# Kernel tuning notes

Hardware: AMD Instinct MI355X
Metric: run time of the kernel (lower is better)

The kernel has to match this reference:

```python
import jax, jax.numpy as jnp
import numpy as np

B, S, H = 1, 2048, 4096
NH, NKV, HD = 32, 8, 128
GROUPS = NH // NKV  # 4
THETA = 10000.0
NEG = -1e9


def setup_inputs() -> dict:
    key = jax.random.key(0)
    k1, k2, k3 = jax.random.split(key, 3)
    hidden_states = jax.random.normal(k1, (B, S, H), dtype=jnp.float32)
    w_qkv = jax.random.normal(k2, (H, (NH + 2 * NKV) * HD), dtype=jnp.float32) * 0.02
    w_o = jax.random.normal(k3, (NH * HD, H), dtype=jnp.float32) * 0.02
    causal = jnp.tril(jnp.ones((S, S), dtype=bool))
    attention_mask = jnp.where(causal, 0.0, NEG).astype(jnp.float32)[None, None]  # [1,1,S,S]
    return {"hidden_states": hidden_states, "w_qkv": w_qkv, "w_o": w_o,
            "attention_mask": attention_mask}


def _rope_freqs(seqlen, head_dim, theta):
    inv = 1.0 / (theta ** (jnp.arange(0, head_dim, 2, dtype=jnp.float32) / head_dim))
    t = jnp.arange(seqlen, dtype=jnp.float32)
    freqs = t[:, None] * inv[None, :]              # [S, HD/2]
    return jnp.cos(freqs), jnp.sin(freqs)


def _apply_rope(x, cos, sin):
    # x: [B,S,heads,HD]; source pairs x[i] with x[i+HD/2] (NeoX rotate-half)
    half = x.shape[-1] // 2
    x1, x2 = x[..., :half], x[..., half:]
    c = cos[None, :, None, :]
    s = sin[None, :, None, :]
    return jnp.concatenate([x1 * c - x2 * s, x1 * s + x2 * c], axis=-1)


def reference(hidden_states, w_qkv, w_o, attention_mask):
    bsz, seqlen, _ = hidden_states.shape
    xqkv = hidden_states @ w_qkv                            # [B,S,(NH+2*NKV)*HD]
    xqkv = xqkv.reshape(bsz, seqlen, NH + 2 * NKV, HD)
    xq = xqkv[:, :, :NH]                                    # [B,S,NH,HD]
    xk = xqkv[:, :, NH:NH + NKV]                            # [B,S,NKV,HD]
    xv = xqkv[:, :, NH + NKV:]                              # [B,S,NKV,HD]

    cos, sin = _rope_freqs(seqlen, HD, THETA)               # start_pos = 0 (prefill)
    xq = _apply_rope(xq, cos, sin)
    xk = _apply_rope(xk, cos, sin)

    # GQA: repeat kv heads to match query heads
    keys = jnp.repeat(xk, GROUPS, axis=2)                   # [B,S,NH,HD]
    values = jnp.repeat(xv, GROUPS, axis=2)

    scores = jnp.einsum('bqhd,bkhd->bhqk', xq, keys) / np.sqrt(HD)
    scores = scores + attention_mask
    probs = jax.nn.softmax(scores.astype(jnp.float32), axis=-1).astype(xq.dtype)
    out = jnp.einsum('bhqk,bkhd->bqhd', probs, values)      # [B,S,NH,HD]
    attention_weight = out.reshape(bsz, seqlen, NH * HD)
    attn_output = attention_weight @ w_o                    # [B,S,H]
    return attn_output
```

## Files before the change

### kernel.cpp

```cpp
#include <hip/hip_runtime.h>

typedef __bf16 bf16_8 __attribute__((ext_vector_type(8)));
typedef float f32x4 __attribute__((ext_vector_type(4)));
typedef unsigned short ushort8v __attribute__((ext_vector_type(8)));
typedef unsigned short ushort4v __attribute__((ext_vector_type(4)));

#define SEQ 2048
#define HDIM 4096
#define NHEADS 32
#define NKVH 8
#define HEADD 128
#define NQKV 6144

__device__ __forceinline__ unsigned short f2bf(float f) {
    unsigned int u = __float_as_uint(f);
    u += 0x7fffu + ((u >> 16) & 1u);
    return (unsigned short)(u >> 16);
}
__device__ __forceinline__ float bf2f(unsigned short v) {
    return __uint_as_float(((unsigned int)v) << 16);
}

#if defined(__has_builtin)
#if __has_builtin(__builtin_amdgcn_exp2f)
#define EXP2(x) __builtin_amdgcn_exp2f(x)
#endif
#endif
#ifndef EXP2
#define EXP2(x) __expf(0.69314718055994531f * (x))
#endif

typedef __attribute__((address_space(1))) void as1_void;
typedef __attribute__((address_space(3))) void as3_void;
__device__ __forceinline__ void gload16(const unsigned short* g, unsigned short* l) {
    __builtin_amdgcn_global_load_lds((as1_void*)g, (as3_void*)l, 16, 0, 0);
}

__global__ void k_f32_to_bf16(const float* __restrict__ in, unsigned short* __restrict__ out, int n) {
    int i = (blockIdx.x * blockDim.x + threadIdx.x) * 4;
    if (i >= n) return;
    float4 v = *reinterpret_cast<const float4*>(in + i);
    ushort4v o = { f2bf(v.x), f2bf(v.y), f2bf(v.z), f2bf(v.w) };
    *reinterpret_cast<ushort4v*>(out + i) = o;
}

__global__ void k_transpose_f32_to_bf16(const float* __restrict__ in, unsigned short* __restrict__ out,
                                        int K, int N) {
    __shared__ unsigned short tile[64][72];
    int k0 = blockIdx.y * 64, n0 = blockIdx.x * 64;
    int t = threadIdx.x;
    int r = t >> 2;
    int cs = (t & 3) * 16;
    int sw = (r >> 4) * 16;
    const float* src = in + (size_t)(k0 + r) * N + n0 + cs;
#pragma unroll
    for (int j = 0; j < 16; j += 4) {
        float4 v = *reinterpret_cast<const float4*>(src + j);
        tile[r][(cs + j + 0) ^ sw] = f2bf(v.x);
        tile[r][(cs + j + 1) ^ sw] = f2bf(v.y);
        tile[r][(cs + j + 2) ^ sw] = f2bf(v.z);
        tile[r][(cs + j + 3) ^ sw] = f2bf(v.w);
    }
    __syncthreads();
    int rr = t >> 2;
    int ks = (t & 3) * 16;
    unsigned short tmp[16];
#pragma unroll
    for (int i = 0; i < 16; i++) tmp[i] = tile[ks + i][rr ^ (((ks + i) >> 4) * 16)];
    unsigned short* dst = out + (size_t)(n0 + rr) * K + k0 + ks;
    *reinterpret_cast<ushort8v*>(dst) = *reinterpret_cast<const ushort8v*>(tmp);
    *reinterpret_cast<ushort8v*>(dst + 8) = *reinterpret_cast<const ushort8v*>(tmp + 8);
}

__global__ void k_transpose_bf16(const unsigned short* __restrict__ in, unsigned short* __restrict__ out,
                                 int inStride, int outStride) {
    __shared__ unsigned short tile[64][72];
    int r0 = blockIdx.y * 64, c0 = blockIdx.x * 64;
    int t = threadIdx.x;
    int r = t >> 2;
    int cs = (t & 3) * 16;
    int csw = cs ^ ((r >> 4) * 16);
    const unsigned short* src = in + (size_t)(r0 + r) * inStride + c0 + cs;
    *reinterpret_cast<ushort8v*>(&tile[r][csw])     = *reinterpret_cast<const ushort8v*>(src);
    *reinterpret_cast<ushort8v*>(&tile[r][csw + 8]) = *reinterpret_cast<const ushort8v*>(src + 8);
    __syncthreads();
    int rr = t >> 2;
    int ks = (t & 3) * 16;
    unsigned short tmp[16];
#pragma unroll
    for (int i = 0; i < 16; i++) tmp[i] = tile[ks + i][rr ^ (((ks + i) >> 4) * 16)];
    unsigned short* dst = out + (size_t)(c0 + rr) * outStride + r0 + ks;
    *reinterpret_cast<ushort8v*>(dst) = *reinterpret_cast<const ushort8v*>(tmp);
    *reinterpret_cast<ushort8v*>(dst + 8) = *reinterpret_cast<const ushort8v*>(tmp + 8);
}


#define STAGE_A(TILE, KH) do { if ((TILE) < NT) {                                        \
    size_t kb_ = (size_t)(TILE) * 128 + (size_t)((KH) * 64);                             \
    gload16((const unsigned short*)(srcA0 + kb_),                                        \
            (unsigned short*)(smem + ((TILE) & 1) * 32768 + (KH) * 16384 + wby));        \
    gload16((const unsigned short*)(srcA1 + kb_),                                        \
            (unsigned short*)(smem + ((TILE) & 1) * 32768 + (KH) * 16384 + 8192 + wby)); \
  } } while (0)

#define STAGE_B(TILE, KH) do { if ((TILE) < NT) {                                        \
    size_t kb_ = (size_t)(TILE) * 128 + (size_t)((KH) * 64);                             \
    gload16((const unsigned short*)(srcB0 + kb_),                                        \
            (unsigned short*)(smem + 65536 + ((TILE) & 1) * 32768 + (KH) * 16384 + wby)); \
    gload16((const unsigned short*)(srcB1 + kb_),                                        \
            (unsigned short*)(smem + 65536 + ((TILE) & 1) * 32768 + (KH) * 16384 + 8192 + wby)); \
  } } while (0)

#define MFMA_ROW(ACCI, AV)                                                                \
    acc[ACCI][0] = __builtin_amdgcn_mfma_f32_16x16x32_bf16(AV, b0, acc[ACCI][0], 0, 0, 0); \
    acc[ACCI][1] = __builtin_amdgcn_mfma_f32_16x16x32_bf16(AV, b1, acc[ACCI][1], 0, 0, 0); \
    acc[ACCI][2] = __builtin_amdgcn_mfma_f32_16x16x32_bf16(AV, b2, acc[ACCI][2], 0, 0, 0); \
    acc[ACCI][3] = __builtin_amdgcn_mfma_f32_16x16x32_bf16(AV, b3, acc[ACCI][3], 0, 0, 0);

#define PHASE(PB, PKH, PMH, DOB, STAGE_STMT, DOVM) do {                                   \
    const char* ab_ = smem + (PB) * 32768 + (PKH) * 16384;                                \
    a0 = *(const bf16_8*)(ab_ + offA[(PMH) * 4 + 0]);                                     \
    a1 = *(const bf16_8*)(ab_ + offA[(PMH) * 4 + 1]);                                     \
    a2 = *(const bf16_8*)(ab_ + offA[(PMH) * 4 + 2]);                                     \
    a3 = *(const bf16_8*)(ab_ + offA[(PMH) * 4 + 3]);                                     \
    if (DOB) {                                                                            \
        const char* bb_ = smem + 65536 + (PB) * 32768 + (PKH) * 16384;                    \
        b0 = *(const bf16_8*)(bb_ + offB[0]);                                             \
        b1 = *(const bf16_8*)(bb_ + offB[1]);                                             \
        b2 = *(const bf16_8*)(bb_ + offB[2]);                                             \
        b3 = *(const bf16_8*)(bb_ + offB[3]);                                             \
    }                                                                                     \
    STAGE_STMT;                                                                           \
    if (DOVM) asm volatile("s_waitcnt vmcnt(8)" ::: "memory");                            \
    __builtin_amdgcn_s_barrier();                                                         \
    __builtin_amdgcn_s_setprio(1);                                                        \
    MFMA_ROW((PMH) * 4 + 0, a0)                                                           \
    MFMA_ROW((PMH) * 4 + 1, a1)                                                           \
    MFMA_ROW((PMH) * 4 + 2, a2)                                                           \
    MFMA_ROW((PMH) * 4 + 3, a3)                                                           \
    __builtin_amdgcn_s_setprio(0);                                                        \
    asm volatile("s_waitcnt lgkmcnt(0)" ::: "memory");                                    \
    __builtin_amdgcn_s_barrier();                                                         \
  } while (0)

template <bool OUT_BF16>
__global__ __launch_bounds__(512, 2) void k_gemm256(
    const unsigned short* __restrict__ A,
    const unsigned short* __restrict__ Bt,
    void* __restrict__ Cv,
    int N, int K)
{
    extern __shared__ char smem[];
    const int NT = K >> 6;
    const int NTN = N >> 8;

    int nwg = gridDim.x;
    int bid = blockIdx.x;
    int cpx = nwg >> 3;
    int sw = (bid & 7) * cpx + (bid >> 3);
    int tm = sw / NTN, tn = sw % NTN;
    int gm0 = tm << 8, gn0 = tn << 8;

    int t = threadIdx.x;
    int w = t >> 6, lane = t & 63;
    int l15 = lane & 15, quad = lane >> 4;
    int wr = w >> 2, wc = w & 3;
    int wby = w << 10;

    int offA[8], offB[4];
#pragma unroll
    for (int mh = 0; mh < 2; mh++)
#pragma unroll
        for (int mi = 0; mi < 4; mi++) {
            int row = wr * 128 + mh * 64 + mi * 16 + l15;
            offA[mh * 4 + mi] = row * 64 + ((quad ^ ((row >> 1) & 3)) << 4);
        }
#pragma unroll
    for (int nj = 0; nj < 4; nj++) {
        int row = wc * 64 + nj * 16 + l15;
        offB[nj] = row * 64 + ((quad ^ ((row >> 1) & 3)) << 4);
    }

    int srow0 = t >> 2;
    int sslot = (t & 3) ^ ((srow0 >> 1) & 3);
    const char* srcA0 = (const char*)A  + ((size_t)(gm0 + srow0)       * K + sslot * 8) * 2;
    const char* srcA1 = (const char*)A  + ((size_t)(gm0 + srow0 + 128) * K + sslot * 8) * 2;
    const char* srcB0 = (const char*)Bt + ((size_t)(gn0 + srow0)       * K + sslot * 8) * 2;
    const char* srcB1 = (const char*)Bt + ((size_t)(gn0 + srow0 + 128) * K + sslot * 8) * 2;

    f32x4 acc[8][4] = {};
    bf16_8 a0, a1, a2, a3, b0, b1, b2, b3;

    STAGE_A(0, 0); STAGE_B(0, 0);
    STAGE_A(0, 1); STAGE_B(0, 1);
    STAGE_A(1, 0); STAGE_B(1, 0);
    asm volatile("s_waitcnt vmcnt(8)" ::: "memory");
    __builtin_amdgcn_s_barrier();

    const int NITER = K >> 7;
    for (int it = 0; it < NITER; ++it) {
        int T1 = 2 * it + 1, T2 = T1 + 1, T3 = T1 + 2;
        PHASE(0, 0, 0, 1, STAGE_A(T1, 1), 0);
        PHASE(0, 0, 1, 0, STAGE_B(T1, 1), 1);
        PHASE(0, 1, 0, 1, STAGE_A(T2, 0), 0);
        PHASE(0, 1, 1, 0, STAGE_B(T2, 0), 1);
        PHASE(1, 0, 0, 1, STAGE_A(T2, 1), 0);
        PHASE(1, 0, 1, 0, STAGE_B(T2, 1), 1);
        PHASE(1, 1, 0, 1, STAGE_A(T3, 0), 0);
        PHASE(1, 1, 1, 0, STAGE_B(T3, 0), 1);
    }

    int crow = gm0 + wr * 128 + quad * 4;
    int ccol = gn0 + wc * 64 + l15;
#pragma unroll
    for (int m8 = 0; m8 < 8; m8++)
#pragma unroll
        for (int nj = 0; nj < 4; nj++)
#pragma unroll
            for (int r = 0; r < 4; r++) {
                size_t idx = (size_t)(crow + m8 * 16 + r) * N + (ccol + nj * 16);
                float v = acc[m8][nj][r];
                if (OUT_BF16) ((unsigned short*)Cv)[idx] = f2bf(v);
                else          ((float*)Cv)[idx] = v;
            }
}

#undef STAGE_A
#undef STAGE_B
#undef MFMA_ROW
#undef PHASE

__global__ void k_rope_split(const unsigned short* __restrict__ qkv,
                             unsigned short* __restrict__ Qb,
                             unsigned short* __restrict__ Kb)
{
    int wid = blockIdx.x * 4 + (threadIdx.x >> 6);
    int lane = threadIdx.x & 63;
    int head = wid % 40;
    int s = wid / 40;
    const unsigned short* src = qkv + (size_t)s * NQKV + head * HEADD;
    float x1 = bf2f(src[lane]);
    float x2 = bf2f(src[lane + 64]);
    float inv = __expf(-(float)lane * 0.14391156831212787f);
    float ang = (float)s * inv;
    float sn, c;
    __sincosf(ang, &sn, &c);
    float o1 = x1 * c - x2 * sn;
    float o2 = x1 * sn + x2 * c;
    unsigned short* dst;
    if (head < 32) {
        const float s2 = 0.12752908270648427f;
        o1 *= s2; o2 *= s2;
        dst = Qb + ((size_t)head * SEQ + s) * HEADD;
    } else {
        dst = Kb + ((size_t)(head - 32) * SEQ + s) * HEADD;
    }
    dst[lane] = f2bf(o1);
    dst[lane + 64] = f2bf(o2);
}

__global__ __launch_bounds__(256, 4) void k_attention(
    const unsigned short* __restrict__ Qb,
    const unsigned short* __restrict__ Kb,
    const unsigned short* __restrict__ Vt,
    unsigned short* __restrict__ Ob)
{
    __shared__ unsigned short Ks[64][136];
    __shared__ unsigned short Vs[128][72];
    __shared__ unsigned short Ps[4][16][72];
    int h  = blockIdx.y;
    int hkv = h >> 2;
    int t = threadIdx.x;
    int w = t >> 6, lane = t & 63, l15 = lane & 15, quad = lane >> 4;

    const unsigned short* kbase = Kb + (size_t)hkv * SEQ * HEADD;
    const unsigned short* vbase = Vt + (size_t)hkv * HEADD * SEQ;

    int qtile[2] = { (int)blockIdx.x, 31 - (int)blockIdx.x };

    for (int ph = 0; ph < 2; ph++) {
        int q0 = qtile[ph] * 64;
        int qm0 = q0 + w * 16;
        int qg = qm0 + l15;

        bf16_8 aq[4];
        {
            const unsigned short* qp = Qb + ((size_t)h * SEQ + qg) * HEADD + quad * 8;
#pragma unroll
            for (int kk = 0; kk < 4; kk++)
                aq[kk] = *reinterpret_cast<const bf16_8*>(qp + kk * 32);
        }

        f32x4 o[8] = {};
        float l_ = 0.f;

        for (int kv0 = 0; kv0 < q0 + 64; kv0 += 64) {
            __syncthreads();
#pragma unroll
            for (int p = 0; p < 4; p++) {
                int r = p * 16 + (t >> 4), c = (t & 15) * 8;
                *reinterpret_cast<ushort8v*>(&Ks[r][c]) =
                    *reinterpret_cast<const ushort8v*>(kbase + (size_t)(kv0 + r) * HEADD + c);
            }
#pragma unroll
            for (int p = 0; p < 4; p++) {
                int r = p * 32 + (t >> 3), c = (t & 7) * 8;
                *reinterpret_cast<ushort8v*>(&Vs[r][c]) =
                    *reinterpret_cast<const ushort8v*>(vbase + (size_t)r * SEQ + kv0 + c);
            }
            __syncthreads();

            if (kv0 > qm0 + 15) continue;

            f32x4 sc[4];
#pragma unroll
            for (int nt = 0; nt < 4; nt++) {
                f32x4 z = {};
#pragma unroll
                for (int kk = 0; kk < 4; kk++) {
                    bf16_8 bk = *reinterpret_cast<const bf16_8*>(&Ks[nt * 16 + l15][kk * 32 + quad * 8]);
                    z = __builtin_amdgcn_mfma_f32_16x16x32_bf16(bk, aq[kk], z, 0, 0, 0);
                }
                sc[nt] = z;
            }
            bool needMask = (kv0 + 63 > qm0);
#pragma unroll
            for (int nt = 0; nt < 4; nt++)
#pragma unroll
                for (int r = 0; r < 4; r++) {
                    float a = sc[nt][r] - 12.0f;
                    if (needMask) {
                        int kg = kv0 + nt * 16 + quad * 4 + r;
                        if (kg > qg) a = -1000.0f;
                    }
                    float p = EXP2(a);
                    sc[nt][r] = p;
                    l_ += p;
                }
#pragma unroll
            for (int nt = 0; nt < 4; nt++) {
                ushort4v pk = { f2bf(sc[nt][0]), f2bf(sc[nt][1]), f2bf(sc[nt][2]), f2bf(sc[nt][3]) };
                *reinterpret_cast<ushort4v*>(&Ps[w][l15][nt * 16 + quad * 4]) = pk;
            }
            asm volatile("s_waitcnt lgkmcnt(0)" ::: "memory");
            bf16_8 pf[2];
#pragma unroll
            for (int kk = 0; kk < 2; kk++)
                pf[kk] = *reinterpret_cast<const bf16_8*>(&Ps[w][l15][kk * 32 + quad * 8]);
#pragma unroll
            for (int dt = 0; dt < 8; dt++)
#pragma unroll
                for (int kk = 0; kk < 2; kk++) {
                    bf16_8 av = *reinterpret_cast<const bf16_8*>(&Vs[dt * 16 + l15][kk * 32 + quad * 8]);
                    o[dt] = __builtin_amdgcn_mfma_f32_16x16x32_bf16(av, pf[kk], o[dt], 0, 0, 0);
                }
        }
        l_ += __shfl_xor(l_, 16, 64);
        l_ += __shfl_xor(l_, 32, 64);
        float rinv = 1.0f / l_;
        unsigned short* orow = Ob + (size_t)qg * (NHEADS * HEADD) + h * HEADD + quad * 4;
#pragma unroll
        for (int dt = 0; dt < 8; dt++) {
            ushort4v pk = { f2bf(o[dt][0] * rinv), f2bf(o[dt][1] * rinv),
                            f2bf(o[dt][2] * rinv), f2bf(o[dt][3] * rinv) };
            *reinterpret_cast<ushort4v*>(orow + dt * 16) = pk;
        }
    }
}

extern "C" void kernel_launch(void* const* d_in, const int* in_sizes, int n_in,
                              void* d_out, int out_size, void* d_ws, size_t ws_size,
                              hipStream_t stream) {
    const float* hs    = (const float*)d_in[0];
    const float* w_qkv = (const float*)d_in[1];
    const float* w_o   = (const float*)d_in[2];

    static bool s_attr_set = false;
    if (!s_attr_set) {
        hipFuncSetAttribute(reinterpret_cast<const void*>(k_gemm256<true>),
                            hipFuncAttributeMaxDynamicSharedMemorySize, 131072);
        hipFuncSetAttribute(reinterpret_cast<const void*>(k_gemm256<false>),
                            hipFuncAttributeMaxDynamicSharedMemorySize, 131072);
        s_attr_set = true;
    }

    char* ws = (char*)d_ws;
    size_t off = 0;
    auto alloc = [&](size_t bytes) -> void* {
        void* p = ws + off;
        off += (bytes + 255) & ~(size_t)255;
        return p;
    };
    unsigned short* Xb    = (unsigned short*)alloc((size_t)SEQ * HDIM * 2);
    unsigned short* R1    = (unsigned short*)alloc((size_t)NQKV * HDIM * 2);
    unsigned short* Wot   = (unsigned short*)alloc((size_t)HDIM * HDIM * 2);
    unsigned short* QKVb  = (unsigned short*)alloc((size_t)SEQ * NQKV * 2);
    unsigned short* Wqkvt = R1;
    unsigned short* Qb = R1;
    unsigned short* Kb = Qb + (size_t)NHEADS * SEQ * HEADD;
    unsigned short* Vt = Kb + (size_t)NKVH * SEQ * HEADD;
    unsigned short* AOb = Xb;

    k_f32_to_bf16<<<(SEQ * HDIM) / 1024, 256, 0, stream>>>(hs, Xb, SEQ * HDIM);
    k_transpose_f32_to_bf16<<<dim3(NQKV / 64, HDIM / 64), 256, 0, stream>>>(w_qkv, Wqkvt, HDIM, NQKV);
    k_transpose_f32_to_bf16<<<dim3(HDIM / 64, HDIM / 64), 256, 0, stream>>>(w_o, Wot, HDIM, HDIM);
    k_gemm256<true><<<dim3((SEQ / 256) * (NQKV / 256)), dim3(512), 131072, stream>>>(
        Xb, Wqkvt, QKVb, NQKV, HDIM);
    k_rope_split<<<(SEQ * 40) / 4, 256, 0, stream>>>(QKVb, Qb, Kb);
    k_transpose_bf16<<<dim3((NKVH * HEADD) / 64, SEQ / 64), 256, 0, stream>>>(
        QKVb + (size_t)(NHEADS + NKVH) * HEADD, Vt, NQKV, SEQ);
    k_attention<<<dim3(16, NHEADS), 256, 0, stream>>>(Qb, Kb, Vt, AOb);
    k_gemm256<false><<<dim3((SEQ / 256) * (HDIM / 256)), dim3(512), 131072, stream>>>(
        AOb, Wot, d_out, HDIM, HDIM);
}
```

Baseline: 546.7 us.

## Fuse W_o transpose into QKV GEMM grid and use 256x128 tiles for output GEMM

```diff
diff --git a/kernel.cpp b/kernel.cpp
--- a/kernel.cpp
+++ b/kernel.cpp
@@ -95,89 +95,131 @@
 }
 
 
+#define RG(BUF, KH) (smem + ((BUF) * 2 + (KH)) * PR)
+
 #define STAGE_A(TILE, KH) do { if ((TILE) < NT) {                                        \
     size_t kb_ = (size_t)(TILE) * 128 + (size_t)((KH) * 64);                             \
-    gload16((const unsigned short*)(srcA0 + kb_),                                        \
-            (unsigned short*)(smem + ((TILE) & 1) * 32768 + (KH) * 16384 + wby));        \
-    gload16((const unsigned short*)(srcA1 + kb_),                                        \
-            (unsigned short*)(smem + ((TILE) & 1) * 32768 + (KH) * 16384 + 8192 + wby)); \
+    char* d_ = RG((TILE) & 1, KH) + wby;                                                 \
+    gload16((const unsigned short*)(srcA0 + kb_), (unsigned short*)d_);                  \
+    gload16((const unsigned short*)(srcA1 + kb_), (unsigned short*)(d_ + 8192));         \
   } } while (0)
 
 #define STAGE_B(TILE, KH) do { if ((TILE) < NT) {                                        \
     size_t kb_ = (size_t)(TILE) * 128 + (size_t)((KH) * 64);                             \
-    gload16((const unsigned short*)(srcB0 + kb_),                                        \
-            (unsigned short*)(smem + 65536 + ((TILE) & 1) * 32768 + (KH) * 16384 + wby)); \
-    gload16((const unsigned short*)(srcB1 + kb_),                                        \
-            (unsigned short*)(smem + 65536 + ((TILE) & 1) * 32768 + (KH) * 16384 + 8192 + wby)); \
+    char* d_ = RG((TILE) & 1, KH) + 16384 + wby;                                         \
+    gload16((const unsigned short*)(srcB0 + kb_), (unsigned short*)d_);                  \
+    if constexpr (BN == 256)                                                             \
+        gload16((const unsigned short*)(srcB1 + kb_), (unsigned short*)(d_ + 8192));     \
   } } while (0)
 
-#define MFMA_ROW(ACCI, AV)                                                                \
-    acc[ACCI][0] = __builtin_amdgcn_mfma_f32_16x16x32_bf16(AV, b0, acc[ACCI][0], 0, 0, 0); \
-    acc[ACCI][1] = __builtin_amdgcn_mfma_f32_16x16x32_bf16(AV, b1, acc[ACCI][1], 0, 0, 0); \
-    acc[ACCI][2] = __builtin_amdgcn_mfma_f32_16x16x32_bf16(AV, b2, acc[ACCI][2], 0, 0, 0); \
-    acc[ACCI][3] = __builtin_amdgcn_mfma_f32_16x16x32_bf16(AV, b3, acc[ACCI][3], 0, 0, 0);
-
-#define PHASE(PB, PKH, PMH, DOB, STAGE_STMT, DOVM) do {                                   \
-    const char* ab_ = smem + (PB) * 32768 + (PKH) * 16384;                                \
-    a0 = *(const bf16_8*)(ab_ + offA[(PMH) * 4 + 0]);                                     \
-    a1 = *(const bf16_8*)(ab_ + offA[(PMH) * 4 + 1]);                                     \
-    a2 = *(const bf16_8*)(ab_ + offA[(PMH) * 4 + 2]);                                     \
-    a3 = *(const bf16_8*)(ab_ + offA[(PMH) * 4 + 3]);                                     \
-    if (DOB) {                                                                            \
-        const char* bb_ = smem + 65536 + (PB) * 32768 + (PKH) * 16384;                    \
-        b0 = *(const bf16_8*)(bb_ + offB[0]);                                             \
-        b1 = *(const bf16_8*)(bb_ + offB[1]);                                             \
-        b2 = *(const bf16_8*)(bb_ + offB[2]);                                             \
-        b3 = *(const bf16_8*)(bb_ + offB[3]);                                             \
-    }                                                                                     \
-    STAGE_STMT;                                                                           \
-    if (DOVM) asm volatile("s_waitcnt vmcnt(8)" ::: "memory");                            \
-    __builtin_amdgcn_s_barrier();                                                         \
-    __builtin_amdgcn_s_setprio(1);                                                        \
-    MFMA_ROW((PMH) * 4 + 0, a0)                                                           \
-    MFMA_ROW((PMH) * 4 + 1, a1)                                                           \
-    MFMA_ROW((PMH) * 4 + 2, a2)                                                           \
-    MFMA_ROW((PMH) * 4 + 3, a3)                                                           \
-    __builtin_amdgcn_s_setprio(0);                                                        \
-    asm volatile("s_waitcnt lgkmcnt(0)" ::: "memory");                                    \
-    __builtin_amdgcn_s_barrier();                                                         \
+#define VMW_N() do {                                                                     \
+    if constexpr (BN == 256) asm volatile("s_waitcnt vmcnt(8)" ::: "memory");            \
+    else                     asm volatile("s_waitcnt vmcnt(6)" ::: "memory");            \
   } while (0)
 
-template <bool OUT_BF16>
+#define TAILVM() do {                                                                    \
+    if (tail) asm volatile("s_waitcnt vmcnt(0)" ::: "memory");                           \
+    else      VMW_N();                                                                   \
+  } while (0)
+
+#define PHASE(PB, PKH, PMH, STAGE_STMT, VM_STMT) do {                                    \
+    const char* ab_ = RG(PB, PKH);                                                       \
+    bf16_8 av_[MF2];                                                                     \
+    _Pragma("unroll")                                                                    \
+    for (int mi_ = 0; mi_ < MF2; ++mi_)                                                  \
+        av_[mi_] = *(const bf16_8*)(ab_ + offA[(PMH) * MF2 + mi_]);                      \
+    if ((PMH) == 0) {                                                                    \
+        _Pragma("unroll")                                                                \
+        for (int nj_ = 0; nj_ < 4; ++nj_)                                                \
+            bv[nj_] = *(const bf16_8*)(ab_ + 16384 + offB[nj_]);                         \
+    }                                                                                    \
+    STAGE_STMT;                                                                          \
+    VM_STMT;                                                                             \
+    __builtin_amdgcn_s_barrier();                                                        \
+    __builtin_amdgcn_s_setprio(1);                                                       \
+    _Pragma("unroll")                                                                    \
+    for (int mi_ = 0; mi_ < MF2; ++mi_) {                                                \
+        _Pragma("unroll")                                                                \
+        for (int nj_ = 0; nj_ < 4; ++nj_)                                                \
+            acc[(PMH) * MF2 + mi_][nj_] = __builtin_amdgcn_mfma_f32_16x16x32_bf16(       \
+                av_[mi_], bv[nj_], acc[(PMH) * MF2 + mi_][nj_], 0, 0, 0);                \
+    }                                                                                    \
+    __builtin_amdgcn_s_setprio(0);                                                       \
+    asm volatile("s_waitcnt lgkmcnt(0)" ::: "memory");                                   \
+    __builtin_amdgcn_s_barrier();                                                        \
+  } while (0)
+
+template <int BN, int WM, int WN, bool OUT_BF16, bool FUSE_T>
 __global__ __launch_bounds__(512, 2) void k_gemm256(
     const unsigned short* __restrict__ A,
     const unsigned short* __restrict__ Bt,
     void* __restrict__ Cv,
-    int N, int K)
+    int N, int K, int nwgemm, int ntn,
+    const float* __restrict__ TPin, unsigned short* __restrict__ TPout)
 {
     extern __shared__ char smem[];
+    constexpr int PWR = 256 / WM;
+    constexpr int PWC = BN / WN;
+    constexpr int MF  = PWR / 16;
+    constexpr int MF2 = MF / 2;
+    constexpr int PR  = 16384 + BN * 64;
+    int t = threadIdx.x;
+
+    if constexpr (FUSE_T) {
+        if ((int)blockIdx.x >= nwgemm) {
+            int tb = blockIdx.x - nwgemm;
+            int half = t >> 8, lt = t & 255;
+            unsigned short* tile = (unsigned short*)smem + half * (64 * 72);
+            int r = lt >> 2, cs = (lt & 3) * 16, sw = (r >> 4) * 16;
+            for (int i = 0; i < 32; ++i) {
+                int tau = tb * 64 + i * 2 + half;
+                int n0 = (tau & 63) * 64, k0 = (tau >> 6) * 64;
+                const float* src = TPin + (size_t)(k0 + r) * 4096 + n0 + cs;
+#pragma unroll
+                for (int j = 0; j < 16; j += 4) {
+                    float4 v = *reinterpret_cast<const float4*>(src + j);
+                    tile[r * 72 + ((cs + j + 0) ^ sw)] = f2bf(v.x);
+                    tile[r * 72 + ((cs + j + 1) ^ sw)] = f2bf(v.y);
+                    tile[r * 72 + ((cs + j + 2) ^ sw)] = f2bf(v.z);
+                    tile[r * 72 + ((cs + j + 3) ^ sw)] = f2bf(v.w);
+                }
+                __syncthreads();
+                unsigned short tmp[16];
+#pragma unroll
+                for (int q = 0; q < 16; q++)
+                    tmp[q] = tile[(cs + q) * 72 + (r ^ (((cs + q) >> 4) * 16))];
+                unsigned short* dst = TPout + (size_t)(n0 + r) * 4096 + k0 + cs;
+                *reinterpret_cast<ushort8v*>(dst) = *reinterpret_cast<const ushort8v*>(tmp);
+                *reinterpret_cast<ushort8v*>(dst + 8) = *reinterpret_cast<const ushort8v*>(tmp + 8);
+                __syncthreads();
+            }
+            return;
+        }
+    }
+
     const int NT = K >> 6;
-    const int NTN = N >> 8;
-
-    int nwg = gridDim.x;
     int bid = blockIdx.x;
-    int cpx = nwg >> 3;
-    int sw = (bid & 7) * cpx + (bid >> 3);
-    int tm = sw / NTN, tn = sw % NTN;
-    int gm0 = tm << 8, gn0 = tn << 8;
-
-    int t = threadIdx.x;
+    int cpx = nwgemm >> 3;
+    int sw_ = (bid & 7) * cpx + (bid >> 3);
+    int tm = sw_ / ntn, tn = sw_ % ntn;
+    int gm0 = tm << 8, gn0 = tn * BN;
+
     int w = t >> 6, lane = t & 63;
     int l15 = lane & 15, quad = lane >> 4;
-    int wr = w >> 2, wc = w & 3;
+    int wr = w / WN, wc = w % WN;
     int wby = w << 10;
 
-    int offA[8], offB[4];
+    int offA[MF], offB[4];
 #pragma unroll
     for (int mh = 0; mh < 2; mh++)
 #pragma unroll
-        for (int mi = 0; mi < 4; mi++) {
-            int row = wr * 128 + mh * 64 + mi * 16 + l15;
-            offA[mh * 4 + mi] = row * 64 + ((quad ^ ((row >> 1) & 3)) << 4);
+        for (int mi = 0; mi < MF2; mi++) {
+            int row = wr * PWR + mh * (PWR / 2) + mi * 16 + l15;
+            offA[mh * MF2 + mi] = row * 64 + ((quad ^ ((row >> 1) & 3)) << 4);
         }
 #pragma unroll
     for (int nj = 0; nj < 4; nj++) {
-        int row = wc * 64 + nj * 16 + l15;
+        int row = wc * PWC + nj * 16 + l15;
         offB[nj] = row * 64 + ((quad ^ ((row >> 1) & 3)) << 4);
     }
 
@@ -186,48 +228,53 @@
     const char* srcA0 = (const char*)A  + ((size_t)(gm0 + srow0)       * K + sslot * 8) * 2;
     const char* srcA1 = (const char*)A  + ((size_t)(gm0 + srow0 + 128) * K + sslot * 8) * 2;
     const char* srcB0 = (const char*)Bt + ((size_t)(gn0 + srow0)       * K + sslot * 8) * 2;
-    const char* srcB1 = (const char*)Bt + ((size_t)(gn0 + srow0 + 128) * K + sslot * 8) * 2;
-
-    f32x4 acc[8][4] = {};
-    bf16_8 a0, a1, a2, a3, b0, b1, b2, b3;
+    const char* srcB1 = (BN == 256)
+        ? (const char*)Bt + ((size_t)(gn0 + srow0 + 128) * K + sslot * 8) * 2
+        : srcB0;
+
+    f32x4 acc[MF][4] = {};
+    bf16_8 bv[4];
 
     STAGE_A(0, 0); STAGE_B(0, 0);
     STAGE_A(0, 1); STAGE_B(0, 1);
     STAGE_A(1, 0); STAGE_B(1, 0);
-    asm volatile("s_waitcnt vmcnt(8)" ::: "memory");
+    VMW_N();
     __builtin_amdgcn_s_barrier();
 
     const int NITER = K >> 7;
     for (int it = 0; it < NITER; ++it) {
         int T1 = 2 * it + 1, T2 = T1 + 1, T3 = T1 + 2;
-        PHASE(0, 0, 0, 1, STAGE_A(T1, 1), 0);
-        PHASE(0, 0, 1, 0, STAGE_B(T1, 1), 1);
-        PHASE(0, 1, 0, 1, STAGE_A(T2, 0), 0);
-        PHASE(0, 1, 1, 0, STAGE_B(T2, 0), 1);
-        PHASE(1, 0, 0, 1, STAGE_A(T2, 1), 0);
-        PHASE(1, 0, 1, 0, STAGE_B(T2, 1), 1);
-        PHASE(1, 1, 0, 1, STAGE_A(T3, 0), 0);
-        PHASE(1, 1, 1, 0, STAGE_B(T3, 0), 1);
-    }
-
-    int crow = gm0 + wr * 128 + quad * 4;
-    int ccol = gn0 + wc * 64 + l15;
-#pragma unroll
-    for (int m8 = 0; m8 < 8; m8++)
+        bool tail = (it == NITER - 1);
+        PHASE(0, 0, 0, STAGE_A(T1, 1), ((void)0));
+        PHASE(0, 0, 1, STAGE_B(T1, 1), VMW_N());
+        PHASE(0, 1, 0, STAGE_A(T2, 0), ((void)0));
+        PHASE(0, 1, 1, STAGE_B(T2, 0), TAILVM());
+        PHASE(1, 0, 0, STAGE_A(T2, 1), ((void)0));
+        PHASE(1, 0, 1, STAGE_B(T2, 1), VMW_N());
+        PHASE(1, 1, 0, STAGE_A(T3, 0), ((void)0));
+        PHASE(1, 1, 1, STAGE_B(T3, 0), VMW_N());
+    }
+
+    int crow = gm0 + wr * PWR + quad * 4;
+    int ccol = gn0 + wc * PWC + l15;
+#pragma unroll
+    for (int m = 0; m < MF; m++)
 #pragma unroll
         for (int nj = 0; nj < 4; nj++)
 #pragma unroll
             for (int r = 0; r < 4; r++) {
-                size_t idx = (size_t)(crow + m8 * 16 + r) * N + (ccol + nj * 16);
-                float v = acc[m8][nj][r];
+                size_t idx = (size_t)(crow + m * 16 + r) * N + (ccol + nj * 16);
+                float v = acc[m][nj][r];
                 if (OUT_BF16) ((unsigned short*)Cv)[idx] = f2bf(v);
                 else          ((float*)Cv)[idx] = v;
             }
 }
 
+#undef RG
 #undef STAGE_A
 #undef STAGE_B
-#undef MFMA_ROW
+#undef VMW_N
+#undef TAILVM
 #undef PHASE
 
 __global__ void k_rope_split(const unsigned short* __restrict__ qkv,
@@ -377,9 +424,9 @@
 
     static bool s_attr_set = false;
     if (!s_attr_set) {
-        hipFuncSetAttribute(reinterpret_cast<const void*>(k_gemm256<true>),
+        hipFuncSetAttribute(reinterpret_cast<const void*>(k_gemm256<256, 2, 4, true, true>),
                             hipFuncAttributeMaxDynamicSharedMemorySize, 131072);
-        hipFuncSetAttribute(reinterpret_cast<const void*>(k_gemm256<false>),
+        hipFuncSetAttribute(reinterpret_cast<const void*>(k_gemm256<128, 4, 2, false, false>),
                             hipFuncAttributeMaxDynamicSharedMemorySize, 131072);
         s_attr_set = true;
     }
@@ -403,13 +450,12 @@
 
     k_f32_to_bf16<<<(SEQ * HDIM) / 1024, 256, 0, stream>>>(hs, Xb, SEQ * HDIM);
     k_transpose_f32_to_bf16<<<dim3(NQKV / 64, HDIM / 64), 256, 0, stream>>>(w_qkv, Wqkvt, HDIM, NQKV);
-    k_transpose_f32_to_bf16<<<dim3(HDIM / 64, HDIM / 64), 256, 0, stream>>>(w_o, Wot, HDIM, HDIM);
-    k_gemm256<true><<<dim3((SEQ / 256) * (NQKV / 256)), dim3(512), 131072, stream>>>(
-        Xb, Wqkvt, QKVb, NQKV, HDIM);
+    k_gemm256<256, 2, 4, true, true><<<dim3(256), dim3(512), 131072, stream>>>(
+        Xb, Wqkvt, QKVb, NQKV, HDIM, 192, NQKV / 256, w_o, Wot);
     k_rope_split<<<(SEQ * 40) / 4, 256, 0, stream>>>(QKVb, Qb, Kb);
     k_transpose_bf16<<<dim3((NKVH * HEADD) / 64, SEQ / 64), 256, 0, stream>>>(
         QKVb + (size_t)(NHEADS + NKVH) * HEADD, Vt, NQKV, SEQ);
     k_attention<<<dim3(16, NHEADS), 256, 0, stream>>>(Qb, Kb, Vt, AOb);
-    k_gemm256<false><<<dim3((SEQ / 256) * (HDIM / 256)), dim3(512), 131072, stream>>>(
-        AOb, Wot, d_out, HDIM, HDIM);
-}
+    k_gemm256<128, 4, 2, false, false><<<dim3(256), dim3(512), 98304, stream>>>(
+        AOb, Wot, d_out, HDIM, HDIM, 256, HDIM / 128, nullptr, nullptr);
+}
```

New measurement: 486.0 us. -11.1%, faster.
